# Performance work log

Measured on AMD Instinct MI355X. Metric: run time of the kernel, lower is better.

## Reference

```python
import jax, jax.numpy as jnp
import numpy as np

NUM_EXPERTS = 8
HIDDEN = 1024
INTERMEDIATE = 4096
TOKENS_PER_EXPERT = 2048


def _init_uniform(key, shape):
    # mirrors init_: uniform(-std, std) with std = 1/sqrt(last_dim)
    std = 1.0 / np.sqrt(shape[-1])
    return jax.random.uniform(key, shape, dtype=jnp.float32, minval=-std, maxval=std)


def setup_inputs() -> dict:
    key = jax.random.key(0)
    kx, k1, k2 = jax.random.split(key, 3)
    x = jax.random.normal(kx, (NUM_EXPERTS, TOKENS_PER_EXPERT, HIDDEN), dtype=jnp.float32)
    w1 = _init_uniform(k1, (NUM_EXPERTS, HIDDEN, INTERMEDIATE))
    w2 = _init_uniform(k2, (NUM_EXPERTS, INTERMEDIATE, HIDDEN))
    return {"x": x, "w1": w1, "w2": w2}


def reference(x, w1, w2):
    # grouped GEMM over experts: [e,n,d] @ [e,d,h] -> [e,n,h]
    hidden = jnp.einsum('end,edh->enh', x, w1)
    hidden = jax.nn.gelu(hidden, approximate=False)  # torch nn.GELU default = exact erf
    out = jnp.einsum('enh,ehd->end', hidden, w2)
    return out
```

## Files before the change

### kernel.cpp

```cpp
#include <hip/hip_runtime.h>
#include <hip/hip_bf16.h>
#include <math.h>

#define NE 8
#define MM 2048
#define DH 1024
#define DI 4096

#define BK  32
#define LDA 40

typedef short bf16x8 __attribute__((ext_vector_type(8)));
typedef float f32x4  __attribute__((ext_vector_type(4)));

__device__ __forceinline__ unsigned short f2bf(float f) {
    unsigned u = __builtin_bit_cast(unsigned, f);
    u += 0x7FFFu + ((u >> 16) & 1u);
    return (unsigned short)(u >> 16);
}

__device__ __forceinline__ void gload_lds16(const void* g, void* l) {
    __builtin_amdgcn_global_load_lds(
        (__attribute__((address_space(1))) void*)g,
        (__attribute__((address_space(3))) void*)l, 16, 0, 0);
}

__global__ __launch_bounds__(256)
void convert_bf16(const float* __restrict__ in, unsigned short* __restrict__ out,
                  long long n)
{
    long long i = ((long long)blockIdx.x * 256 + threadIdx.x) * 8;
    const float4 v0 = *(const float4*)(in + i);
    const float4 v1 = *(const float4*)(in + i + 4);
    bf16x8 s;
    s[0] = (short)f2bf(v0.x); s[1] = (short)f2bf(v0.y);
    s[2] = (short)f2bf(v0.z); s[3] = (short)f2bf(v0.w);
    s[4] = (short)f2bf(v1.x); s[5] = (short)f2bf(v1.y);
    s[6] = (short)f2bf(v1.z); s[7] = (short)f2bf(v1.w);
    *(bf16x8*)(out + i) = s;
}

__global__ __launch_bounds__(256)
void transpose_bf16(const float* __restrict__ in, unsigned short* __restrict__ out,
                    int K, int N)
{
    __shared__ short tile[64][66];
    const int e  = blockIdx.z;
    const int n0 = blockIdx.x * 64;
    const int k0 = blockIdx.y * 64;
    const float* ine = in + (size_t)e * K * N;
    unsigned short* oute = out + (size_t)e * N * K;
    const int tid = threadIdx.x;

    #pragma unroll
    for (int i = 0; i < 4; ++i) {
        int idx = tid + i * 256;
        int r  = idx >> 4;
        int c  = (idx & 15) * 4;
        const float4 v = *(const float4*)(ine + (size_t)(k0 + r) * N + n0 + c);
        tile[r][c + 0] = (short)f2bf(v.x);
        tile[r][c + 1] = (short)f2bf(v.y);
        tile[r][c + 2] = (short)f2bf(v.z);
        tile[r][c + 3] = (short)f2bf(v.w);
    }
    __syncthreads();
    #pragma unroll
    for (int i = 0; i < 4; ++i) {
        int idx = tid + i * 256;
        int n  = idx >> 4;
        int k  = (idx & 15) * 4;
        short4 s;
        s.x = tile[k + 0][n];
        s.y = tile[k + 1][n];
        s.z = tile[k + 2][n];
        s.w = tile[k + 3][n];
        *(short4*)(oute + (size_t)(n0 + n) * K + k0 + k) = s;
    }
}

#define GEMM_PROLOG(Kdim)                                                      \
    __shared__ short As[128 * 32];                                             \
    __shared__ short Bs[128 * 32];                                             \
    const int tid  = threadIdx.x;                                              \
    const int lane = tid & 63;                                                 \
    const int wave = tid >> 6;                                                 \
    const int wm = (wave >> 1) * 64;                                           \
    const int wn = (wave &  1) * 64;                                           \
    const int lr = lane & 15;                                                  \
    const int lq = lane >> 4;                                                  \
    f32x4 acc[4][4] = {};                                                      \
    for (int k0 = 0; k0 < (Kdim); k0 += BK) {                                  \
        _Pragma("unroll")                                                      \
        for (int i = 0; i < 2; ++i) {                                          \
            int idx = tid + i * 256;                                           \
            int row = idx >> 2;                                                \
            int col = (idx & 3) * 8;                                           \
            gload_lds16(Ae + (size_t)(m0 + row) * (Kdim) + k0 + col,           \
                        As + (i * 256 + wave * 64) * 8);                       \
            gload_lds16(Be + (size_t)(n0 + row) * (Kdim) + k0 + col,           \
                        Bs + (i * 256 + wave * 64) * 8);                       \
        }                                                                      \
        __syncthreads();                                                       \
        bf16x8 a[4], b[4];                                                     \
        _Pragma("unroll")                                                      \
        for (int i = 0; i < 4; ++i)                                            \
            a[i] = *(const bf16x8*)(&As[(wm + i * 16 + lr) * 32 + lq * 8]);    \
        _Pragma("unroll")                                                      \
        for (int i = 0; i < 4; ++i)                                            \
            b[i] = *(const bf16x8*)(&Bs[(wn + i * 16 + lr) * 32 + lq * 8]);    \
        _Pragma("unroll")                                                      \
        for (int mi = 0; mi < 4; ++mi)                                         \
            _Pragma("unroll")                                                  \
            for (int ni = 0; ni < 4; ++ni)                                     \
                acc[mi][ni] = __builtin_amdgcn_mfma_f32_16x16x32_bf16(         \
                    a[mi], b[ni], acc[mi][ni], 0, 0, 0);                       \
        __syncthreads();                                                       \
    }

__global__ __launch_bounds__(256, 2)
void gemm1_bf16(const unsigned short* __restrict__ Xb,
                const unsigned short* __restrict__ W1t,
                unsigned short* __restrict__ H)
{
    const int e  = blockIdx.z;
    const int m0 = blockIdx.y * 128;
    const int n0 = blockIdx.x * 128;
    const unsigned short* Ae = Xb  + (size_t)e * MM * DH;
    const unsigned short* Be = W1t + (size_t)e * DI * DH;
    unsigned short* He = H + (size_t)e * MM * DI;

    GEMM_PROLOG(DH)

    #pragma unroll
    for (int mi = 0; mi < 4; ++mi) {
        #pragma unroll
        for (int ni = 0; ni < 4; ++ni) {
            const int col = n0 + wn + ni * 16 + lr;
            #pragma unroll
            for (int r = 0; r < 4; ++r) {
                const int row = m0 + wm + mi * 16 + lq * 4 + r;
                float v = acc[mi][ni][r];
                float g = 0.5f * v * (1.0f + erff(v * 0.70710678118654752f));
                He[(size_t)row * DI + col] = f2bf(g);
            }
        }
    }
}

__global__ __launch_bounds__(256, 2)
void gemm2_bf16(const unsigned short* __restrict__ H,
                const unsigned short* __restrict__ W2t,
                float* __restrict__ O)
{
    const int e  = blockIdx.z;
    const int m0 = blockIdx.y * 128;
    const int n0 = blockIdx.x * 128;
    const unsigned short* Ae = H   + (size_t)e * MM * DI;
    const unsigned short* Be = W2t + (size_t)e * DH * DI;
    float* Oe = O + (size_t)e * MM * DH;

    GEMM_PROLOG(DI)

    #pragma unroll
    for (int mi = 0; mi < 4; ++mi) {
        #pragma unroll
        for (int ni = 0; ni < 4; ++ni) {
            const int col = n0 + wn + ni * 16 + lr;
            #pragma unroll
            for (int r = 0; r < 4; ++r) {
                const int row = m0 + wm + mi * 16 + lq * 4 + r;
                Oe[(size_t)row * DH + col] = acc[mi][ni][r];
            }
        }
    }
}

__global__ __launch_bounds__(256, 2)
void gemm1_mixed(const float* __restrict__ X, const unsigned short* __restrict__ W1t,
                 unsigned short* __restrict__ H)
{
    __shared__ short As[128 * LDA];
    __shared__ short Bs[128 * 32];
    const int e  = blockIdx.z;
    const int m0 = blockIdx.y * 128;
    const int n0 = blockIdx.x * 128;
    const float* Xe = X + (size_t)e * MM * DH;
    const unsigned short* Bt = W1t + (size_t)e * DI * DH;
    unsigned short* He = H + (size_t)e * MM * DI;
    const int tid  = threadIdx.x;
    const int lane = tid & 63;
    const int wave = tid >> 6;
    const int wm = (wave >> 1) * 64;
    const int wn = (wave &  1) * 64;
    const int lr = lane & 15;
    const int lq = lane >> 4;
    f32x4 acc[4][4] = {};
    for (int k0 = 0; k0 < DH; k0 += BK) {
        #pragma unroll
        for (int i = 0; i < 2; ++i) {
            int idx  = tid + i * 256;
            gload_lds16(Bt + (size_t)(n0 + (idx >> 2)) * DH + k0 + (idx & 3) * 8,
                        Bs + (i * 256 + wave * 64) * 8);
        }
        #pragma unroll
        for (int i = 0; i < 4; ++i) {
            int idx = tid + i * 256;
            int row = idx >> 3;
            int col = (idx & 7) * 4;
            const float4 v = *(const float4*)(Xe + (size_t)(m0 + row) * DH + k0 + col);
            short4 s;
            s.x = (short)f2bf(v.x); s.y = (short)f2bf(v.y);
            s.z = (short)f2bf(v.z); s.w = (short)f2bf(v.w);
            *(short4*)(&As[row * LDA + col]) = s;
        }
        __syncthreads();
        bf16x8 a[4], b[4];
        #pragma unroll
        for (int i = 0; i < 4; ++i)
            a[i] = *(const bf16x8*)(&As[(wm + i * 16 + lr) * LDA + lq * 8]);
        #pragma unroll
        for (int i = 0; i < 4; ++i)
            b[i] = *(const bf16x8*)(&Bs[(wn + i * 16 + lr) * 32 + lq * 8]);
        #pragma unroll
        for (int mi = 0; mi < 4; ++mi)
            #pragma unroll
            for (int ni = 0; ni < 4; ++ni)
                acc[mi][ni] = __builtin_amdgcn_mfma_f32_16x16x32_bf16(a[mi], b[ni], acc[mi][ni], 0, 0, 0);
        __syncthreads();
    }
    #pragma unroll
    for (int mi = 0; mi < 4; ++mi) {
        #pragma unroll
        for (int ni = 0; ni < 4; ++ni) {
            const int col = n0 + wn + ni * 16 + lr;
            #pragma unroll
            for (int r = 0; r < 4; ++r) {
                const int row = m0 + wm + mi * 16 + lq * 4 + r;
                float v = acc[mi][ni][r];
                float g = 0.5f * v * (1.0f + erff(v * 0.70710678118654752f));
                He[(size_t)row * DI + col] = f2bf(g);
            }
        }
    }
}

__global__ __launch_bounds__(256, 2)
void fb_gemm1(const float* __restrict__ X, const float* __restrict__ W1,
              unsigned short* __restrict__ H)
{
    __shared__ short As[128 * LDA];
    __shared__ short Bs[128 * LDA];
    const int e  = blockIdx.z;
    const int m0 = blockIdx.y * 128;
    const int n0 = blockIdx.x * 128;
    const float* Xe  = X  + (size_t)e * MM * DH;
    const float* W1e = W1 + (size_t)e * DH * DI;
    unsigned short* He = H + (size_t)e * MM * DI;
    const int tid  = threadIdx.x;
    const int lane = tid & 63;
    const int wave = tid >> 6;
    const int wm = (wave >> 1) * 64;
    const int wn = (wave &  1) * 64;
    const int lr = lane & 15;
    const int lq = lane >> 4;
    f32x4 acc[4][4] = {};
    for (int k0 = 0; k0 < DH; k0 += BK) {
        #pragma unroll
        for (int i = 0; i < 4; ++i) {
            int idx = tid + i * 256;
            int row = idx >> 3;
            int col = (idx & 7) * 4;
            const float4 v = *(const float4*)(Xe + (size_t)(m0 + row) * DH + k0 + col);
            short4 s;
            s.x = (short)f2bf(v.x); s.y = (short)f2bf(v.y);
            s.z = (short)f2bf(v.z); s.w = (short)f2bf(v.w);
            *(short4*)(&As[row * LDA + col]) = s;
        }
        #pragma unroll
        for (int i = 0; i < 4; ++i) {
            int idx  = tid + i * 256;
            int krow = idx >> 5;
            int ncol = (idx & 31) * 4;
            const float4 v = *(const float4*)(W1e + (size_t)(k0 + krow) * DI + n0 + ncol);
            Bs[(ncol + 0) * LDA + krow] = (short)f2bf(v.x);
            Bs[(ncol + 1) * LDA + krow] = (short)f2bf(v.y);
            Bs[(ncol + 2) * LDA + krow] = (short)f2bf(v.z);
            Bs[(ncol + 3) * LDA + krow] = (short)f2bf(v.w);
        }
        __syncthreads();
        bf16x8 a[4], b[4];
        #pragma unroll
        for (int i = 0; i < 4; ++i)
            a[i] = *(const bf16x8*)(&As[(wm + i * 16 + lr) * LDA + lq * 8]);
        #pragma unroll
        for (int i = 0; i < 4; ++i)
            b[i] = *(const bf16x8*)(&Bs[(wn + i * 16 + lr) * LDA + lq * 8]);
        #pragma unroll
        for (int mi = 0; mi < 4; ++mi)
            #pragma unroll
            for (int ni = 0; ni < 4; ++ni)
                acc[mi][ni] = __builtin_amdgcn_mfma_f32_16x16x32_bf16(a[mi], b[ni], acc[mi][ni], 0, 0, 0);
        __syncthreads();
    }
    #pragma unroll
    for (int mi = 0; mi < 4; ++mi) {
        #pragma unroll
        for (int ni = 0; ni < 4; ++ni) {
            const int col = n0 + wn + ni * 16 + lr;
            #pragma unroll
            for (int r = 0; r < 4; ++r) {
                const int row = m0 + wm + mi * 16 + lq * 4 + r;
                float v = acc[mi][ni][r];
                float g = 0.5f * v * (1.0f + erff(v * 0.70710678118654752f));
                He[(size_t)row * DI + col] = f2bf(g);
            }
        }
    }
}

__global__ __launch_bounds__(256, 2)
void fb_gemm2(const unsigned short* __restrict__ H, const float* __restrict__ W2,
              float* __restrict__ O)
{
    __shared__ short As[128 * LDA];
    __shared__ short Bs[128 * LDA];
    const int e  = blockIdx.z;
    const int m0 = blockIdx.y * 128;
    const int n0 = blockIdx.x * 128;
    const unsigned short* He = H + (size_t)e * MM * DI;
    const float* W2e = W2 + (size_t)e * DI * DH;
    float* Oe = O + (size_t)e * MM * DH;
    const int tid  = threadIdx.x;
    const int lane = tid & 63;
    const int wave = tid >> 6;
    const int wm = (wave >> 1) * 64;
    const int wn = (wave &  1) * 64;
    const int lr = lane & 15;
    const int lq = lane >> 4;
    f32x4 acc[4][4] = {};
    for (int k0 = 0; k0 < DI; k0 += BK) {
        #pragma unroll
        for (int i = 0; i < 2; ++i) {
            int idx = tid + i * 256;
            int row = idx >> 2;
            int col = (idx & 3) * 8;
            bf16x8 v = *(const bf16x8*)(He + (size_t)(m0 + row) * DI + k0 + col);
            *(bf16x8*)(&As[row * LDA + col]) = v;
        }
        #pragma unroll
        for (int i = 0; i < 4; ++i) {
            int idx  = tid + i * 256;
            int krow = idx >> 5;
            int ncol = (idx & 31) * 4;
            const float4 v = *(const float4*)(W2e + (size_t)(k0 + krow) * DH + n0 + ncol);
            Bs[(ncol + 0) * LDA + krow] = (short)f2bf(v.x);
            Bs[(ncol + 1) * LDA + krow] = (short)f2bf(v.y);
            Bs[(ncol + 2) * LDA + krow] = (short)f2bf(v.z);
            Bs[(ncol + 3) * LDA + krow] = (short)f2bf(v.w);
        }
        __syncthreads();
        bf16x8 a[4], b[4];
        #pragma unroll
        for (int i = 0; i < 4; ++i)
            a[i] = *(const bf16x8*)(&As[(wm + i * 16 + lr) * LDA + lq * 8]);
        #pragma unroll
        for (int i = 0; i < 4; ++i)
            b[i] = *(const bf16x8*)(&Bs[(wn + i * 16 + lr) * LDA + lq * 8]);
        #pragma unroll
        for (int mi = 0; mi < 4; ++mi)
            #pragma unroll
            for (int ni = 0; ni < 4; ++ni)
                acc[mi][ni] = __builtin_amdgcn_mfma_f32_16x16x32_bf16(a[mi], b[ni], acc[mi][ni], 0, 0, 0);
        __syncthreads();
    }
    #pragma unroll
    for (int mi = 0; mi < 4; ++mi) {
        #pragma unroll
        for (int ni = 0; ni < 4; ++ni) {
            const int col = n0 + wn + ni * 16 + lr;
            #pragma unroll
            for (int r = 0; r < 4; ++r) {
                const int row = m0 + wm + mi * 16 + lq * 4 + r;
                Oe[(size_t)row * DH + col] = acc[mi][ni][r];
            }
        }
    }
}

extern "C" void kernel_launch(void* const* d_in, const int* in_sizes, int n_in,
                              void* d_out, int out_size, void* d_ws, size_t ws_size,
                              hipStream_t stream) {
    const float* x  = (const float*)d_in[0];
    const float* w1 = (const float*)d_in[1];
    const float* w2 = (const float*)d_in[2];
    float* out = (float*)d_out;

    const size_t WT_BYTES     = (size_t)NE * DH * DI * 2;
    const size_t HIDDEN_BYTES = (size_t)NE * MM * DI * 2;
    const size_t XB_BYTES     = (size_t)NE * MM * DH * 2;

    dim3 blk(256);
    if (ws_size >= WT_BYTES + HIDDEN_BYTES + XB_BYTES) {
        unsigned short* wt     = (unsigned short*)d_ws;
        unsigned short* hidden = (unsigned short*)((char*)d_ws + WT_BYTES);
        unsigned short* xb     = (unsigned short*)((char*)d_ws + WT_BYTES + HIDDEN_BYTES);
        const long long nx = (long long)NE * MM * DH;
        convert_bf16<<<dim3((unsigned)(nx / (8 * 256))), blk, 0, stream>>>(x, xb, nx);
        transpose_bf16<<<dim3(DI / 64, DH / 64, NE), blk, 0, stream>>>(w1, wt, DH, DI);
        gemm1_bf16<<<dim3(DI / 128, MM / 128, NE), blk, 0, stream>>>(xb, wt, hidden);
        transpose_bf16<<<dim3(DH / 64, DI / 64, NE), blk, 0, stream>>>(w2, wt, DI, DH);
        gemm2_bf16<<<dim3(DH / 128, MM / 128, NE), blk, 0, stream>>>(hidden, wt, out);
    } else if (ws_size >= WT_BYTES + HIDDEN_BYTES) {
        unsigned short* wt     = (unsigned short*)d_ws;
        unsigned short* hidden = (unsigned short*)((char*)d_ws + WT_BYTES);
        transpose_bf16<<<dim3(DI / 64, DH / 64, NE), blk, 0, stream>>>(w1, wt, DH, DI);
        gemm1_mixed<<<dim3(DI / 128, MM / 128, NE), blk, 0, stream>>>(x, wt, hidden);
        transpose_bf16<<<dim3(DH / 64, DI / 64, NE), blk, 0, stream>>>(w2, wt, DI, DH);
        gemm2_bf16<<<dim3(DH / 128, MM / 128, NE), blk, 0, stream>>>(hidden, wt, out);
    } else {
        unsigned short* hidden = (unsigned short*)d_ws;
        fb_gemm1<<<dim3(DI / 128, MM / 128, NE), blk, 0, stream>>>(x, w1, hidden);
        fb_gemm2<<<dim3(DH / 128, MM / 128, NE), blk, 0, stream>>>(hidden, w2, out);
    }
}
```

Baseline: 723.1 us.

## Double K-tile to 64 with XOR-swizzled LDS and XCD-aware block mapping

Raises the GEMM K step from 32 to 64, so each barrier pair now covers two MFMA sub-steps and half as many synchronizations are needed. Global-to-LDS loads are placed with an XOR swizzle on 16-byte segments to avoid LDS bank conflicts on the fragment reads. The grid is flattened to 1D and remapped so consecutive tiles of the same expert land on the same XCD, improving L2 reuse. The cost is doubled LDS per block (32 KB), which could limit occupancy.

```diff
diff --git a/kernel.cpp b/kernel.cpp
--- a/kernel.cpp
+++ b/kernel.cpp
@@ -78,9 +78,9 @@
     }
 }
 
-#define GEMM_PROLOG(Kdim)                                                      \
-    __shared__ short As[128 * 32];                                             \
-    __shared__ short Bs[128 * 32];                                             \
+#define GEMM_BODY_V2(Kdim)                                                     \
+    __shared__ short As[128 * 64];                                             \
+    __shared__ short Bs[128 * 64];                                             \
     const int tid  = threadIdx.x;                                              \
     const int lane = tid & 63;                                                 \
     const int wave = tid >> 6;                                                 \
@@ -89,47 +89,57 @@
     const int lr = lane & 15;                                                  \
     const int lq = lane >> 4;                                                  \
     f32x4 acc[4][4] = {};                                                      \
-    for (int k0 = 0; k0 < (Kdim); k0 += BK) {                                  \
+    for (int k0 = 0; k0 < (Kdim); k0 += 64) {                                  \
         _Pragma("unroll")                                                      \
-        for (int i = 0; i < 2; ++i) {                                          \
+        for (int i = 0; i < 4; ++i) {                                          \
             int idx = tid + i * 256;                                           \
-            int row = idx >> 2;                                                \
-            int col = (idx & 3) * 8;                                           \
-            gload_lds16(Ae + (size_t)(m0 + row) * (Kdim) + k0 + col,           \
+            int row = idx >> 3;                                                \
+            int gs  = (idx & 7) ^ (row & 7);                                   \
+            gload_lds16(Ae + (size_t)(m0 + row) * (Kdim) + k0 + gs * 8,        \
                         As + (i * 256 + wave * 64) * 8);                       \
-            gload_lds16(Be + (size_t)(n0 + row) * (Kdim) + k0 + col,           \
+            gload_lds16(Be + (size_t)(n0 + row) * (Kdim) + k0 + gs * 8,        \
                         Bs + (i * 256 + wave * 64) * 8);                       \
         }                                                                      \
         __syncthreads();                                                       \
-        bf16x8 a[4], b[4];                                                     \
         _Pragma("unroll")                                                      \
-        for (int i = 0; i < 4; ++i)                                            \
-            a[i] = *(const bf16x8*)(&As[(wm + i * 16 + lr) * 32 + lq * 8]);    \
-        _Pragma("unroll")                                                      \
-        for (int i = 0; i < 4; ++i)                                            \
-            b[i] = *(const bf16x8*)(&Bs[(wn + i * 16 + lr) * 32 + lq * 8]);    \
-        _Pragma("unroll")                                                      \
-        for (int mi = 0; mi < 4; ++mi)                                         \
+        for (int ks = 0; ks < 2; ++ks) {                                       \
+            bf16x8 a[4], b[4];                                                 \
+            const int sl = ((ks * 4 + lq) ^ (lr & 7)) * 8;                     \
             _Pragma("unroll")                                                  \
-            for (int ni = 0; ni < 4; ++ni)                                     \
-                acc[mi][ni] = __builtin_amdgcn_mfma_f32_16x16x32_bf16(         \
-                    a[mi], b[ni], acc[mi][ni], 0, 0, 0);                       \
+            for (int i = 0; i < 4; ++i) {                                      \
+                a[i] = *(const bf16x8*)(&As[(wm + i * 16 + lr) * 64 + sl]);    \
+                b[i] = *(const bf16x8*)(&Bs[(wn + i * 16 + lr) * 64 + sl]);    \
+            }                                                                  \
+            _Pragma("unroll")                                                  \
+            for (int mi = 0; mi < 4; ++mi)                                     \
+                _Pragma("unroll")                                              \
+                for (int ni = 0; ni < 4; ++ni)                                 \
+                    acc[mi][ni] = __builtin_amdgcn_mfma_f32_16x16x32_bf16(     \
+                        a[mi], b[ni], acc[mi][ni], 0, 0, 0);                   \
+        }                                                                      \
         __syncthreads();                                                       \
     }
 
+#define DECOMPOSE_XCD(MB, NB)                                                  \
+    const int nwg   = NE * (MB) * (NB);                                        \
+    const int chunk = nwg >> 3;                                                \
+    int bsw = (blockIdx.x & 7) * chunk + (blockIdx.x >> 3);                    \
+    const int e  = bsw / ((MB) * (NB));                                        \
+    int trem = bsw - e * ((MB) * (NB));                                        \
+    const int m0 = (trem / (NB)) * 128;                                        \
+    const int n0 = (trem - (trem / (NB)) * (NB)) * 128;
+
 __global__ __launch_bounds__(256, 2)
-void gemm1_bf16(const unsigned short* __restrict__ Xb,
-                const unsigned short* __restrict__ W1t,
-                unsigned short* __restrict__ H)
-{
-    const int e  = blockIdx.z;
-    const int m0 = blockIdx.y * 128;
-    const int n0 = blockIdx.x * 128;
+void gemm1_v2(const unsigned short* __restrict__ Xb,
+              const unsigned short* __restrict__ W1t,
+              unsigned short* __restrict__ H)
+{
+    DECOMPOSE_XCD(MM / 128, DI / 128)
     const unsigned short* Ae = Xb  + (size_t)e * MM * DH;
     const unsigned short* Be = W1t + (size_t)e * DI * DH;
     unsigned short* He = H + (size_t)e * MM * DI;
 
-    GEMM_PROLOG(DH)
+    GEMM_BODY_V2(DH)
 
     #pragma unroll
     for (int mi = 0; mi < 4; ++mi) {
@@ -148,18 +158,16 @@
 }
 
 __global__ __launch_bounds__(256, 2)
-void gemm2_bf16(const unsigned short* __restrict__ H,
-                const unsigned short* __restrict__ W2t,
-                float* __restrict__ O)
-{
-    const int e  = blockIdx.z;
-    const int m0 = blockIdx.y * 128;
-    const int n0 = blockIdx.x * 128;
+void gemm2_v2(const unsigned short* __restrict__ H,
+              const unsigned short* __restrict__ W2t,
+              float* __restrict__ O)
+{
+    DECOMPOSE_XCD(MM / 128, DH / 128)
     const unsigned short* Ae = H   + (size_t)e * MM * DI;
     const unsigned short* Be = W2t + (size_t)e * DH * DI;
     float* Oe = O + (size_t)e * MM * DH;
 
-    GEMM_PROLOG(DI)
+    GEMM_BODY_V2(DI)
 
     #pragma unroll
     for (int mi = 0; mi < 4; ++mi) {
@@ -407,16 +415,16 @@
         const long long nx = (long long)NE * MM * DH;
         convert_bf16<<<dim3((unsigned)(nx / (8 * 256))), blk, 0, stream>>>(x, xb, nx);
         transpose_bf16<<<dim3(DI / 64, DH / 64, NE), blk, 0, stream>>>(w1, wt, DH, DI);
-        gemm1_bf16<<<dim3(DI / 128, MM / 128, NE), blk, 0, stream>>>(xb, wt, hidden);
+        gemm1_v2<<<dim3(NE * (MM / 128) * (DI / 128)), blk, 0, stream>>>(xb, wt, hidden);
         transpose_bf16<<<dim3(DH / 64, DI / 64, NE), blk, 0, stream>>>(w2, wt, DI, DH);
-        gemm2_bf16<<<dim3(DH / 128, MM / 128, NE), blk, 0, stream>>>(hidden, wt, out);
+        gemm2_v2<<<dim3(NE * (MM / 128) * (DH / 128)), blk, 0, stream>>>(hidden, wt, out);
     } else if (ws_size >= WT_BYTES + HIDDEN_BYTES) {
         unsigned short* wt     = (unsigned short*)d_ws;
         unsigned short* hidden = (unsigned short*)((char*)d_ws + WT_BYTES);
         transpose_bf16<<<dim3(DI / 64, DH / 64, NE), blk, 0, stream>>>(w1, wt, DH, DI);
         gemm1_mixed<<<dim3(DI / 128, MM / 128, NE), blk, 0, stream>>>(x, wt, hidden);
         transpose_bf16<<<dim3(DH / 64, DI / 64, NE), blk, 0, stream>>>(w2, wt, DI, DH);
-        gemm2_bf16<<<dim3(DH / 128, MM / 128, NE), blk, 0, stream>>>(hidden, wt, out);
+        gemm2_v2<<<dim3(NE * (MM / 128) * (DH / 128)), blk, 0, stream>>>(hidden, wt, out);
     } else {
         unsigned short* hidden = (unsigned short*)d_ws;
         fb_gemm1<<<dim3(DI / 128, MM / 128, NE), blk, 0, stream>>>(x, w1, hidden);
```

Result: faster. 680.4 us (-5.9%).

## Rewrite grouped GEMMs as 256x256 double-buffered pipelined kernels with swizzled LDS

Applied to the files above, without the earlier changes.

Replaces the 128x128, BK=32 GEMM kernels with 512-thread, 256x256-tile kernels. They use BK=64 double-buffered LDS staging with an XOR swizzle to avoid bank conflicts, and explicit vmcnt/barrier scheduling with setprio around the MFMA phases. Blocks are remapped so each XCD works on one expert's tiles for L2 reuse. The exact erf GELU is replaced by an Abramowitz-Stegun polynomial approximation with a fast exp, which reduces epilogue cost at a small accuracy cost. The larger tiles raise arithmetic intensity but use much more LDS and registers per block, and the hand-written wait counts must match the number of in-flight loads.

```diff
diff --git a/kernel.cpp b/kernel.cpp
--- a/kernel.cpp
+++ b/kernel.cpp
@@ -23,6 +23,16 @@
     __builtin_amdgcn_global_load_lds(
         (__attribute__((address_space(1))) void*)g,
         (__attribute__((address_space(3))) void*)l, 16, 0, 0);
+}
+
+__device__ __forceinline__ float gelu_fast(float x) {
+    float z = fabsf(x) * 0.70710678118654752f;
+    float t = __builtin_amdgcn_rcpf(1.0f + 0.3275911f * z);
+    float p = t * (0.254829592f + t * (-0.284496736f + t * (1.421413741f +
+              t * (-1.453152027f + t * 1.061405429f))));
+    float er = 1.0f - p * __expf(-z * z);
+    er = (x < 0.0f) ? -er : er;
+    return 0.5f * x * (1.0f + er);
 }
 
 __global__ __launch_bounds__(256)
@@ -78,97 +88,149 @@
     }
 }
 
-#define GEMM_PROLOG(Kdim)                                                      \
-    __shared__ short As[128 * 32];                                             \
-    __shared__ short Bs[128 * 32];                                             \
+
+#define VMC(n)  asm volatile("s_waitcnt vmcnt(" #n ")" ::: "memory")
+#define LGKM0   do { asm volatile("s_waitcnt lgkmcnt(0)" ::: "memory"); \
+                     __builtin_amdgcn_sched_barrier(0); } while (0)
+#define BARX    do { __builtin_amdgcn_s_barrier(); \
+                     __builtin_amdgcn_sched_barrier(0); } while (0)
+#define PRIO1   __builtin_amdgcn_s_setprio(1)
+#define PRIO0   __builtin_amdgcn_s_setprio(0)
+
+#define STAGE(Ptr, r0, s, t, KD, DstArr)                                       \
+    { const size_t kk = (size_t)(t) * 64;                                      \
+      _Pragma("unroll")                                                        \
+      for (int j = 0; j < 4; ++j) {                                            \
+          int idx = tid + j * 512;                                             \
+          int row = idx >> 3;                                                  \
+          int gs  = (idx & 7) ^ (row & 7);                                     \
+          gload_lds16(Ptr + (size_t)((r0) + row) * (KD) + kk + gs * 8,         \
+                      &DstArr[s][(j * 512 + wave * 64) * 8]); } }
+
+#define LOAD_A(s, h)                                                           \
+    _Pragma("unroll")                                                          \
+    for (int mi = 0; mi < 4; ++mi) {                                           \
+        int r = wm2 * 128 + (h) * 64 + mi * 16 + lr;                           \
+        _Pragma("unroll")                                                      \
+        for (int ks = 0; ks < 2; ++ks)                                         \
+            a[mi][ks] = *(const bf16x8*)(&As[s][r * 64 +                       \
+                          (((ks * 4 + lq) ^ (lr & 7)) * 8)]);                  \
+    }
+
+#define LOAD_B(s)                                                              \
+    _Pragma("unroll")                                                          \
+    for (int ni = 0; ni < 4; ++ni) {                                           \
+        int r = wn4 * 64 + ni * 16 + lr;                                       \
+        _Pragma("unroll")                                                      \
+        for (int ks = 0; ks < 2; ++ks)                                         \
+            b[ni][ks] = *(const bf16x8*)(&Bs[s][r * 64 +                       \
+                          (((ks * 4 + lq) ^ (lr & 7)) * 8)]);                  \
+    }
+
+#define MFMA_HALF(h)                                                           \
+    _Pragma("unroll")                                                          \
+    for (int mi = 0; mi < 4; ++mi)                                             \
+        _Pragma("unroll")                                                      \
+        for (int ni = 0; ni < 4; ++ni)                                         \
+            _Pragma("unroll")                                                  \
+            for (int ks = 0; ks < 2; ++ks)                                     \
+                acc[(h) * 4 + mi][ni] = __builtin_amdgcn_mfma_f32_16x16x32_bf16( \
+                    a[mi][ks], b[ni][ks], acc[(h) * 4 + mi][ni], 0, 0, 0);
+
+#define PIPE_BODY(KD)                                                          \
+    __shared__ short As[2][256 * 64];                                          \
+    __shared__ short Bs[2][256 * 64];                                          \
     const int tid  = threadIdx.x;                                              \
     const int lane = tid & 63;                                                 \
     const int wave = tid >> 6;                                                 \
-    const int wm = (wave >> 1) * 64;                                           \
-    const int wn = (wave &  1) * 64;                                           \
-    const int lr = lane & 15;                                                  \
-    const int lq = lane >> 4;                                                  \
-    f32x4 acc[4][4] = {};                                                      \
-    for (int k0 = 0; k0 < (Kdim); k0 += BK) {                                  \
-        _Pragma("unroll")                                                      \
-        for (int i = 0; i < 2; ++i) {                                          \
-            int idx = tid + i * 256;                                           \
-            int row = idx >> 2;                                                \
-            int col = (idx & 3) * 8;                                           \
-            gload_lds16(Ae + (size_t)(m0 + row) * (Kdim) + k0 + col,           \
-                        As + (i * 256 + wave * 64) * 8);                       \
-            gload_lds16(Be + (size_t)(n0 + row) * (Kdim) + k0 + col,           \
-                        Bs + (i * 256 + wave * 64) * 8);                       \
-        }                                                                      \
-        __syncthreads();                                                       \
-        bf16x8 a[4], b[4];                                                     \
-        _Pragma("unroll")                                                      \
-        for (int i = 0; i < 4; ++i)                                            \
-            a[i] = *(const bf16x8*)(&As[(wm + i * 16 + lr) * 32 + lq * 8]);    \
-        _Pragma("unroll")                                                      \
-        for (int i = 0; i < 4; ++i)                                            \
-            b[i] = *(const bf16x8*)(&Bs[(wn + i * 16 + lr) * 32 + lq * 8]);    \
-        _Pragma("unroll")                                                      \
-        for (int mi = 0; mi < 4; ++mi)                                         \
-            _Pragma("unroll")                                                  \
-            for (int ni = 0; ni < 4; ++ni)                                     \
-                acc[mi][ni] = __builtin_amdgcn_mfma_f32_16x16x32_bf16(         \
-                    a[mi], b[ni], acc[mi][ni], 0, 0, 0);                       \
-        __syncthreads();                                                       \
-    }
-
-__global__ __launch_bounds__(256, 2)
-void gemm1_bf16(const unsigned short* __restrict__ Xb,
-                const unsigned short* __restrict__ W1t,
-                unsigned short* __restrict__ H)
-{
-    const int e  = blockIdx.z;
-    const int m0 = blockIdx.y * 128;
-    const int n0 = blockIdx.x * 128;
+    const int wm2  = wave >> 2;                                                \
+    const int wn4  = wave & 3;                                                 \
+    const int lr   = lane & 15;                                                \
+    const int lq   = lane >> 4;                                                \
+    const int NI   = (KD) / 128;                                               \
+    f32x4 acc[8][4] = {};                                                      \
+    bf16x8 a[4][2], b[4][2];                                                   \
+    STAGE(Ae, m0, 0, 0, KD, As); STAGE(Be, n0, 0, 0, KD, Bs);                  \
+    STAGE(Be, n0, 1, 1, KD, Bs);                                               \
+    VMC(4); BARX;                                                              \
+    _Pragma("unroll 1")                                                        \
+    for (int i = 0; i < NI; ++i) {                                             \
+        const bool nl = (i < NI - 1);                                          \
+                                                  \
+        STAGE(Ae, m0, 1, 2 * i + 1, KD, As);                                   \
+        LOAD_B(0); LOAD_A(0, 0);                                               \
+        LGKM0; PRIO1; MFMA_HALF(0); PRIO0; BARX;                               \
+                                                  \
+        if (nl) STAGE(Be, n0, 0, 2 * i + 2, KD, Bs);                           \
+        LOAD_A(0, 1);                                                          \
+        LGKM0; PRIO1; MFMA_HALF(1); PRIO0;                                     \
+        if (nl) { VMC(4); } else { VMC(0); }                                   \
+        BARX;                                                                  \
+                                                  \
+        if (nl) STAGE(Ae, m0, 0, 2 * i + 2, KD, As);                           \
+        LOAD_B(1); LOAD_A(1, 0);                                               \
+        LGKM0; PRIO1; MFMA_HALF(0); PRIO0; BARX;                               \
+                                                  \
+        if (nl) STAGE(Be, n0, 1, 2 * i + 3, KD, Bs);                           \
+        LOAD_A(1, 1);                                                          \
+        LGKM0; PRIO1; MFMA_HALF(1); PRIO0;                                     \
+        if (nl) VMC(4);                                                        \
+        BARX;                                                                  \
+    }
+
+#define DECOMPOSE_XCD_V3(TPE)                                                  \
+    const int bsw  = (blockIdx.x & 7) * (TPE) + (blockIdx.x >> 3);             \
+    const int e    = bsw / (TPE);                                              \
+    const int trem = bsw - e * (TPE);                                          \
+    const int m0   = (trem & 7) * 256;                                         \
+    const int n0   = (trem >> 3) * 256;
+
+__global__ __launch_bounds__(512, 2)
+void gemm1_v3(const unsigned short* __restrict__ Xb,
+              const unsigned short* __restrict__ W1t,
+              unsigned short* __restrict__ H)
+{
+    DECOMPOSE_XCD_V3(128)
     const unsigned short* Ae = Xb  + (size_t)e * MM * DH;
     const unsigned short* Be = W1t + (size_t)e * DI * DH;
     unsigned short* He = H + (size_t)e * MM * DI;
 
-    GEMM_PROLOG(DH)
-
-    #pragma unroll
-    for (int mi = 0; mi < 4; ++mi) {
+    PIPE_BODY(DH)
+
+    #pragma unroll
+    for (int mi = 0; mi < 8; ++mi) {
         #pragma unroll
         for (int ni = 0; ni < 4; ++ni) {
-            const int col = n0 + wn + ni * 16 + lr;
+            const int col = n0 + wn4 * 64 + ni * 16 + lr;
             #pragma unroll
             for (int r = 0; r < 4; ++r) {
-                const int row = m0 + wm + mi * 16 + lq * 4 + r;
-                float v = acc[mi][ni][r];
-                float g = 0.5f * v * (1.0f + erff(v * 0.70710678118654752f));
-                He[(size_t)row * DI + col] = f2bf(g);
+                const int row = m0 + wm2 * 128 + mi * 16 + lq * 4 + r;
+                He[(size_t)row * DI + col] = f2bf(gelu_fast(acc[mi][ni][r]));
             }
         }
     }
 }
 
-__global__ __launch_bounds__(256, 2)
-void gemm2_bf16(const unsigned short* __restrict__ H,
-                const unsigned short* __restrict__ W2t,
-                float* __restrict__ O)
-{
-    const int e  = blockIdx.z;
-    const int m0 = blockIdx.y * 128;
-    const int n0 = blockIdx.x * 128;
+__global__ __launch_bounds__(512, 2)
+void gemm2_v3(const unsigned short* __restrict__ H,
+              const unsigned short* __restrict__ W2t,
+              float* __restrict__ O)
+{
+    DECOMPOSE_XCD_V3(32)
     const unsigned short* Ae = H   + (size_t)e * MM * DI;
     const unsigned short* Be = W2t + (size_t)e * DH * DI;
     float* Oe = O + (size_t)e * MM * DH;
 
-    GEMM_PROLOG(DI)
-
-    #pragma unroll
-    for (int mi = 0; mi < 4; ++mi) {
+    PIPE_BODY(DI)
+
+    #pragma unroll
+    for (int mi = 0; mi < 8; ++mi) {
         #pragma unroll
         for (int ni = 0; ni < 4; ++ni) {
-            const int col = n0 + wn + ni * 16 + lr;
+            const int col = n0 + wn4 * 64 + ni * 16 + lr;
             #pragma unroll
             for (int r = 0; r < 4; ++r) {
-                const int row = m0 + wm + mi * 16 + lq * 4 + r;
+                const int row = m0 + wm2 * 128 + mi * 16 + lq * 4 + r;
                 Oe[(size_t)row * DH + col] = acc[mi][ni][r];
             }
         }
@@ -236,9 +298,7 @@
             #pragma unroll
             for (int r = 0; r < 4; ++r) {
                 const int row = m0 + wm + mi * 16 + lq * 4 + r;
-                float v = acc[mi][ni][r];
-                float g = 0.5f * v * (1.0f + erff(v * 0.70710678118654752f));
-                He[(size_t)row * DI + col] = f2bf(g);
+                He[(size_t)row * DI + col] = f2bf(gelu_fast(acc[mi][ni][r]));
             }
         }
     }
@@ -310,9 +370,7 @@
             #pragma unroll
             for (int r = 0; r < 4; ++r) {
                 const int row = m0 + wm + mi * 16 + lq * 4 + r;
-                float v = acc[mi][ni][r];
-                float g = 0.5f * v * (1.0f + erff(v * 0.70710678118654752f));
-                He[(size_t)row * DI + col] = f2bf(g);
+                He[(size_t)row * DI + col] = f2bf(gelu_fast(acc[mi][ni][r]));
             }
         }
     }
@@ -399,7 +457,7 @@
     const size_t HIDDEN_BYTES = (size_t)NE * MM * DI * 2;
     const size_t XB_BYTES     = (size_t)NE * MM * DH * 2;
 
-    dim3 blk(256);
+    dim3 blk(256), blk512(512);
     if (ws_size >= WT_BYTES + HIDDEN_BYTES + XB_BYTES) {
         unsigned short* wt     = (unsigned short*)d_ws;
         unsigned short* hidden = (unsigned short*)((char*)d_ws + WT_BYTES);
@@ -407,16 +465,16 @@
         const long long nx = (long long)NE * MM * DH;
         convert_bf16<<<dim3((unsigned)(nx / (8 * 256))), blk, 0, stream>>>(x, xb, nx);
         transpose_bf16<<<dim3(DI / 64, DH / 64, NE), blk, 0, stream>>>(w1, wt, DH, DI);
-        gemm1_bf16<<<dim3(DI / 128, MM / 128, NE), blk, 0, stream>>>(xb, wt, hidden);
+        gemm1_v3<<<dim3(NE * (MM / 256) * (DI / 256)), blk512, 0, stream>>>(xb, wt, hidden);
         transpose_bf16<<<dim3(DH / 64, DI / 64, NE), blk, 0, stream>>>(w2, wt, DI, DH);
-        gemm2_bf16<<<dim3(DH / 128, MM / 128, NE), blk, 0, stream>>>(hidden, wt, out);
+        gemm2_v3<<<dim3(NE * (MM / 256) * (DH / 256)), blk512, 0, stream>>>(hidden, wt, out);
     } else if (ws_size >= WT_BYTES + HIDDEN_BYTES) {
         unsigned short* wt     = (unsigned short*)d_ws;
         unsigned short* hidden = (unsigned short*)((char*)d_ws + WT_BYTES);
         transpose_bf16<<<dim3(DI / 64, DH / 64, NE), blk, 0, stream>>>(w1, wt, DH, DI);
         gemm1_mixed<<<dim3(DI / 128, MM / 128, NE), blk, 0, stream>>>(x, wt, hidden);
         transpose_bf16<<<dim3(DH / 64, DI / 64, NE), blk, 0, stream>>>(w2, wt, DI, DH);
-        gemm2_bf16<<<dim3(DH / 128, MM / 128, NE), blk, 0, stream>>>(hidden, wt, out);
+        gemm2_v3<<<dim3(NE * (MM / 256) * (DH / 256)), blk512, 0, stream>>>(hidden, wt, out);
     } else {
         unsigned short* hidden = (unsigned short*)d_ws;
         fb_gemm1<<<dim3(DI / 128, MM / 128, NE), blk, 0, stream>>>(x, w1, hidden);
```

New measurement: 640.3 us. 11.5% less time.
